# Performance work log

Measured on AMD Instinct MI355X. Metric: run time of the kernel, lower is better.

The kernel has to match this reference:

```python
import jax, jax.numpy as jnp
import numpy as np

N_EMB = 1024
EMB_DIM = 256
COMMITMENT_COST = 0.25


def setup_inputs() -> dict:
    key = jax.random.key(0)
    k1, k2 = jax.random.split(key)
    B = 65536
    x = jax.random.normal(k1, (B, EMB_DIM), dtype=jnp.float32)
    init_bound = 1.0 / 512
    embedding = jax.random.uniform(k2, (N_EMB, EMB_DIM), dtype=jnp.float32,
                                   minval=-init_bound, maxval=init_bound)
    return {"x": x, "embedding": embedding}


def reference(x, embedding):
    B, D = x.shape
    M = embedding.shape[0]
    x_flat = jax.lax.stop_gradient(x)
    # distances[b,m] = ||x_b||^2 + ||e_m||^2 - 2 x_b . e_m  (torch.addmm form)
    distances = (jnp.sum(embedding ** 2, axis=1)[None, :]
                 + jnp.sum(x_flat ** 2, axis=1, keepdims=True)
                 - 2.0 * x_flat @ embedding.T)
    indices = jnp.argmin(distances.astype(jnp.float32), axis=-1)  # [B] int
    quantized = embedding[indices]  # [B, D]

    # commitment loss (quantized detached), masked by non-padding rows
    e_latent = jnp.mean((x - jax.lax.stop_gradient(quantized)) ** 2, axis=-1)  # [B]
    nonpadding = (jnp.sum(jnp.abs(x), axis=-1) > 0).astype(x.dtype)
    loss = COMMITMENT_COST * jnp.sum(e_latent * nonpadding) / jnp.sum(nonpadding)

    # straight-through estimator
    quantized_st = x + jax.lax.stop_gradient(quantized - x)

    # perplexity: avg one-hot probs via bincount (scatter-add, no BxM one-hot)
    counts = jnp.zeros((M,), dtype=jnp.float32).at[indices].add(1.0)
    avg_probs = counts / B
    perplexity = jnp.exp(-jnp.sum(avg_probs * jnp.log(avg_probs + 1e-10)))

    return quantized_st, loss, indices, perplexity
```

## Files before the change

### kernel.cpp

```cpp
#include <hip/hip_runtime.h>

#define BROWS 65536
#define DDIM 256
#define MCODES 1024
#define FLAG_MARGIN 3e-4f
#define RGRP 16
#define NPART 1024

typedef __attribute__((ext_vector_type(8))) _Float16 h8f16;
typedef __attribute__((ext_vector_type(4))) float float4v;

__device__ inline unsigned short f2h_bits(float f) {
  union { _Float16 h; unsigned short u; } cv;
  cv.h = (_Float16)f;
  return cv.u;
}

__global__ __launch_bounds__(256)
void prep_kernel(const float* __restrict__ emb,
                 float* __restrict__ enorm,
                 float* __restrict__ counts, int* __restrict__ nflag,
                 float* __restrict__ loss_extra,
                 unsigned short* __restrict__ eimg, float* __restrict__ embT) {
  int b = blockIdx.x;
  int tid = threadIdx.x;
  if (b < 64) {
    int t = b * 256 + tid;
    if (t < MCODES) counts[t] = 0.0f;
    if (t == 0) *nflag = 0;
    if (t < 2) loss_extra[t] = 0.0f;
    int row = t >> 4;
    int lane = t & 15;
    const float* p = emb + (size_t)row * DDIM;
    int half = (lane >> 3) & 1;
    int j = lane & 7;
    const float* q = p + half * 128 + j;
    float v = q[0];
    float acc = __fmul_rn(v, v);
    #pragma unroll
    for (int i = 1; i < 16; ++i) {
      v = q[i * 8];
      acc = __fadd_rn(acc, __fmul_rn(v, v));
    }
    float o;
    o = __shfl_xor(acc, 1, 64); acc = __fadd_rn(acc, o);
    o = __shfl_xor(acc, 2, 64); acc = __fadd_rn(acc, o);
    o = __shfl_xor(acc, 4, 64); acc = __fadd_rn(acc, o);
    o = __shfl_xor(acc, 8, 64); acc = __fadd_rn(acc, o);
    if (lane == 0) enorm[row] = acc;
  } else if (b < 192) {
    int t = (b - 64) * 256 + tid;
    int lane = t & 63;
    int tile = (t >> 6) & 1;
    int kstep = (t >> 7) & 7;
    int cc = t >> 10;
    int code = cc * 32 + tile * 16 + (lane & 15);
    int kb = kstep * 32 + (lane >> 4) * 8;
    const float* src = emb + (size_t)code * DDIM + kb;
    union { unsigned short u[8]; uint4 v; } out;
    #pragma unroll
    for (int jj = 0; jj < 8; ++jj) out.u[jj] = f2h_bits(src[jj] * 256.0f);
    ((uint4*)eimg)[t] = out.v;
  } else {
    int t = (b - 192) * 256 + tid;
    int base = t * 4;
    int k = base >> 10;
    int m = base & 1023;
    float4 v;
    v.x = emb[(size_t)(m + 0) * DDIM + k];
    v.y = emb[(size_t)(m + 1) * DDIM + k];
    v.z = emb[(size_t)(m + 2) * DDIM + k];
    v.w = emb[(size_t)(m + 3) * DDIM + k];
    *(float4*)&embT[base] = v;
  }
}

__global__ __launch_bounds__(256, 4)
void score_kernel(const float* __restrict__ x, const float* __restrict__ emb,
                  const float* __restrict__ enorm_g,
                  const unsigned short* __restrict__ eimg,
                  int* __restrict__ idx_out, float* __restrict__ out_idxf,
                  float* __restrict__ qout, float* __restrict__ counts,
                  float* __restrict__ loss_part, float* __restrict__ np_part,
                  int* __restrict__ nflag, int* __restrict__ flist) {
  __shared__ __align__(16) unsigned short ebuf[2][8192];
  __shared__ float enorm_s[MCODES];
  __shared__ int lcount;
  __shared__ int lbase;
  __shared__ int lrows[64];
  __shared__ int sidx[64];
  __shared__ unsigned char sflag[64];
  __shared__ float red[8];

  int tid = threadIdx.x;
  int w = tid >> 6;
  int lane = tid & 63;
  int quad = lane >> 4;
  int rowBase = blockIdx.x * 64;
  int waveRow = rowBase + w * 16;

  if (tid == 0) lcount = 0;
  for (int i = tid; i < MCODES; i += 256) enorm_s[i] = enorm_g[i];

  h8f16 xh[8];
  const float* xbase = x + (size_t)(waveRow + (lane & 15)) * DDIM + quad * 8;
  #pragma unroll
  for (int ks = 0; ks < 8; ++ks) {
    const float4* p = (const float4*)(xbase + ks * 32);
    float4 v0 = p[0], v1 = p[1];
    h8f16 h;
    h[0] = (_Float16)v0.x; h[1] = (_Float16)v0.y;
    h[2] = (_Float16)v0.z; h[3] = (_Float16)v0.w;
    h[4] = (_Float16)v1.x; h[5] = (_Float16)v1.y;
    h[6] = (_Float16)v1.z; h[7] = (_Float16)v1.w;
    xh[ks] = h;
  }

  float b1[4], b2[4];
  int i1[4];
  #pragma unroll
  for (int reg = 0; reg < 4; ++reg) { b1[reg] = 3.4e38f; b2[reg] = 3.4e38f; i1[reg] = 0; }

  #define STAGE_CC(ccv, bf) do { \
    const unsigned short* g_ = eimg + (size_t)(ccv) * 8192 + w * 2048 + lane * 8; \
    unsigned short* l_ = &ebuf[(bf)][w * 2048]; \
    _Pragma("unroll") \
    for (int j_ = 0; j_ < 4; ++j_) { \
      __builtin_amdgcn_global_load_lds((const __attribute__((address_space(1))) unsigned int*)(g_ + j_ * 512), \
                                       (__attribute__((address_space(3))) unsigned int*)(l_ + j_ * 512), 16, 0, 0); \
    } \
  } while (0)

  STAGE_CC(0, 0);

  for (int cc = 0; cc < 32; ++cc) {
    int buf = cc & 1;
    __syncthreads();
    if (cc < 31) STAGE_CC(cc + 1, buf ^ 1);

    float4v acc0 = (float4v){0.f, 0.f, 0.f, 0.f};
    float4v acc1 = (float4v){0.f, 0.f, 0.f, 0.f};
    #pragma unroll
    for (int ks = 0; ks < 8; ++ks) {
      h8f16 e0 = *(const h8f16*)&ebuf[buf][ks * 1024 + lane * 8];
      h8f16 e1 = *(const h8f16*)&ebuf[buf][ks * 1024 + 512 + lane * 8];
      acc0 = __builtin_amdgcn_mfma_f32_16x16x32_f16(xh[ks], e0, acc0, 0, 0, 0);
      acc1 = __builtin_amdgcn_mfma_f32_16x16x32_f16(xh[ks], e1, acc1, 0, 0, 0);
    }

    #pragma unroll
    for (int t2 = 0; t2 < 2; ++t2) {
      int m = cc * 32 + t2 * 16 + (lane & 15);
      float en = enorm_s[m];
      #pragma unroll
      for (int reg = 0; reg < 4; ++reg) {
        float av = t2 ? acc1[reg] : acc0[reg];
        float s = __fadd_rn(en, __fmul_rn(-0.0078125f, av));
        if (s < b1[reg]) { b2[reg] = b1[reg]; b1[reg] = s; i1[reg] = m; }
        else { b2[reg] = fminf(b2[reg], s); }
      }
    }
  }

  #pragma unroll
  for (int off = 1; off < 16; off <<= 1) {
    #pragma unroll
    for (int reg = 0; reg < 4; ++reg) {
      float ob1 = __shfl_xor(b1[reg], off, 64);
      float ob2 = __shfl_xor(b2[reg], off, 64);
      int oi = __shfl_xor(i1[reg], off, 64);
      float cb1 = b1[reg], cb2 = b2[reg];
      int ci = i1[reg];
      float nb1, nb2; int ni;
      if (ob1 < cb1)      { nb1 = ob1; ni = oi; nb2 = fminf(cb1, ob2); }
      else if (cb1 < ob1) { nb1 = cb1; ni = ci; nb2 = fminf(ob1, cb2); }
      else                { nb1 = cb1; ni = min(ci, oi); nb2 = cb1; }
      b1[reg] = nb1; b2[reg] = nb2; i1[reg] = ni;
    }
  }

  if ((lane & 15) == 0) {
    #pragma unroll
    for (int reg = 0; reg < 4; ++reg) {
      int row = waveRow + quad * 4 + reg;
      int bi = i1[reg];
      idx_out[row] = bi;
      out_idxf[row] = (float)bi;
      int lr = row - rowBase;
      sidx[lr] = bi;
      int fl = (__fadd_rn(b2[reg], -b1[reg]) <= FLAG_MARGIN) ? 1 : 0;
      sflag[lr] = (unsigned char)fl;
      if (fl) {
        int pp = atomicAdd(&lcount, 1);
        lrows[pp] = row;
      }
    }
  }
  __syncthreads();
  if (tid == 0 && lcount > 0) lbase = atomicAdd(nflag, lcount);
  __syncthreads();
  if (tid < lcount) flist[lbase + tid] = lrows[tid];

  float lsum = 0.0f, nsum = 0.0f;
  for (int it = 0; it < 16; ++it) {
    int lr = w * 16 + it;
    int row = rowBase + lr;
    int id = sidx[lr];
    int fl = sflag[lr];
    float4 xv = ((const float4*)x)[(size_t)row * 64 + lane];
    float4 ev = ((const float4*)emb)[(size_t)id * 64 + lane];
    float4 q;
    q.x = __fadd_rn(xv.x, __fadd_rn(ev.x, -xv.x));
    q.y = __fadd_rn(xv.y, __fadd_rn(ev.y, -xv.y));
    q.z = __fadd_rn(xv.z, __fadd_rn(ev.z, -xv.z));
    q.w = __fadd_rn(xv.w, __fadd_rn(ev.w, -xv.w));
    ((float4*)qout)[(size_t)row * 64 + lane] = q;

    float d0 = xv.x - ev.x, d1 = xv.y - ev.y, d2 = xv.z - ev.z, d3 = xv.w - ev.w;
    float loc = d0 * d0 + d1 * d1 + d2 * d2 + d3 * d3;
    float la = fabsf(xv.x) + fabsf(xv.y) + fabsf(xv.z) + fabsf(xv.w);
    #pragma unroll
    for (int off = 32; off > 0; off >>= 1) {
      loc += __shfl_xor(loc, off, 64);
      la += __shfl_xor(la, off, 64);
    }
    if (lane == 0 && !fl) {
      float np = (la > 0.0f) ? 1.0f : 0.0f;
      lsum += (loc * (1.0f / 256.0f)) * np;
      nsum += np;
      atomicAdd(&counts[id], 1.0f);
    }
  }
  if (lane == 0) { red[w] = lsum; red[4 + w] = nsum; }
  __syncthreads();
  if (tid == 0) {
    loss_part[blockIdx.x] = (red[0] + red[1]) + (red[2] + red[3]);
    np_part[blockIdx.x] = (red[4] + red[5]) + (red[6] + red[7]);
  }
  #undef STAGE_CC
}

__global__ __launch_bounds__(256)
void rescore_kernel(const float* __restrict__ x, const float* __restrict__ emb,
                    const float* __restrict__ embT,
                    const float* __restrict__ enorm,
                    int* __restrict__ idx_out, float* __restrict__ out_idxf,
                    float* __restrict__ qout, float* __restrict__ counts,
                    float* __restrict__ loss_extra,
                    const int* __restrict__ nflag, const int* __restrict__ flist) {
  __shared__ float xs[RGRP][DDIM];
  __shared__ float xnr[RGRP];
  __shared__ int rown[RGRP];
  __shared__ int sbf[RGRP];
  __shared__ float rv[RGRP][256];
  __shared__ int ri[RGRP][256];
  int tid = threadIdx.x;
  int n = nflag[0];

  for (int g = blockIdx.x; g * RGRP < n; g += 1024) {
    int base = g * RGRP;
    int cnt = min(RGRP, n - base);
    __syncthreads();
    if (tid < RGRP) {
      int rr = flist[base + min(tid, cnt - 1)];
      rown[tid] = rr;
    }
    __syncthreads();
    #pragma unroll
    for (int r = 0; r < RGRP; ++r) xs[r][tid] = x[(size_t)rown[r] * DDIM + tid];
    __syncthreads();

    {
      int r = tid >> 4;
      int lane = tid & 15;
      int half = (lane >> 3) & 1;
      int j = lane & 7;
      const float* q = &xs[r][half * 128 + j];
      float v = q[0];
      float acc = __fmul_rn(v, v);
      #pragma unroll
      for (int i = 1; i < 16; ++i) {
        v = q[i * 8];
        acc = __fadd_rn(acc, __fmul_rn(v, v));
      }
      float o;
      o = __shfl_xor(acc, 1, 64); acc = __fadd_rn(acc, o);
      o = __shfl_xor(acc, 2, 64); acc = __fadd_rn(acc, o);
      o = __shfl_xor(acc, 4, 64); acc = __fadd_rn(acc, o);
      o = __shfl_xor(acc, 8, 64); acc = __fadd_rn(acc, o);
      if (lane == 0) xnr[r] = acc;
    }
    __syncthreads();

    float d[4][RGRP];
    #pragma unroll
    for (int c4 = 0; c4 < 4; ++c4)
      #pragma unroll
      for (int r = 0; r < RGRP; ++r) d[c4][r] = 0.0f;

    float e_cur[4][4], e_nxt[4][4];
    #pragma unroll
    for (int kk = 0; kk < 4; ++kk)
      #pragma unroll
      for (int c4 = 0; c4 < 4; ++c4)
        e_cur[kk][c4] = embT[(size_t)kk * 1024 + c4 * 256 + tid];

    for (int k0 = 0; k0 < DDIM; k0 += 4) {
      if (k0 + 4 < DDIM) {
        #pragma unroll
        for (int kk = 0; kk < 4; ++kk)
          #pragma unroll
          for (int c4 = 0; c4 < 4; ++c4)
            e_nxt[kk][c4] = embT[(size_t)(k0 + 4 + kk) * 1024 + c4 * 256 + tid];
      }
      #pragma unroll
      for (int r = 0; r < RGRP; ++r) {
        float4 xv = *(const float4*)&xs[r][k0];
        #pragma unroll
        for (int c4 = 0; c4 < 4; ++c4) {
          d[c4][r] = fmaf(xv.x, e_cur[0][c4], d[c4][r]);
          d[c4][r] = fmaf(xv.y, e_cur[1][c4], d[c4][r]);
          d[c4][r] = fmaf(xv.z, e_cur[2][c4], d[c4][r]);
          d[c4][r] = fmaf(xv.w, e_cur[3][c4], d[c4][r]);
        }
      }
      #pragma unroll
      for (int kk = 0; kk < 4; ++kk)
        #pragma unroll
        for (int c4 = 0; c4 < 4; ++c4)
          e_cur[kk][c4] = e_nxt[kk][c4];
    }

    float b[RGRP]; int bi[RGRP];
    #pragma unroll
    for (int r = 0; r < RGRP; ++r) { b[r] = 3.4e38f; bi[r] = 0; }
    #pragma unroll
    for (int c4 = 0; c4 < 4; ++c4) {
      int m = c4 * 256 + tid;
      float en = enorm[m];
      #pragma unroll
      for (int r = 0; r < RGRP; ++r) {
        float T = __fadd_rn(en, xnr[r]);
        float s = __fadd_rn(T, __fmul_rn(-2.0f, d[c4][r]));
        if (s < b[r] || (s == b[r] && m < bi[r])) { b[r] = s; bi[r] = m; }
      }
    }
    #pragma unroll
    for (int r = 0; r < RGRP; ++r) { rv[r][tid] = b[r]; ri[r][tid] = bi[r]; }
    __syncthreads();
    for (int st = 128; st > 0; st >>= 1) {
      if (tid < st) {
        #pragma unroll
        for (int r = 0; r < RGRP; ++r) {
          float v = rv[r][tid + st]; int m2 = ri[r][tid + st];
          if (v < rv[r][tid] || (v == rv[r][tid] && m2 < ri[r][tid])) { rv[r][tid] = v; ri[r][tid] = m2; }
        }
      }
      __syncthreads();
    }

    if (tid < RGRP) sbf[tid] = ri[tid][0];
    __syncthreads();

    float* laf = (float*)ri;
    #pragma unroll
    for (int r = 0; r < RGRP; ++r) {
      int bf = sbf[r];
      float xv = xs[r][tid];
      float ev = emb[(size_t)bf * DDIM + tid];
      if (r < cnt) {
        float q = __fadd_rn(xv, __fadd_rn(ev, -xv));
        qout[(size_t)rown[r] * DDIM + tid] = q;
      }
      float dd = xv - ev;
      rv[r][tid] = dd * dd;
      laf[r * 256 + tid] = fabsf(xv);
    }
    __syncthreads();
    for (int st = 128; st > 0; st >>= 1) {
      if (tid < st) {
        #pragma unroll
        for (int r = 0; r < RGRP; ++r) {
          rv[r][tid] += rv[r][tid + st];
          laf[r * 256 + tid] += laf[r * 256 + tid + st];
        }
      }
      __syncthreads();
    }
    if (tid < cnt) {
      int bfin = sbf[tid];
      int row = rown[tid];
      float np = (laf[tid * 256] > 0.0f) ? 1.0f : 0.0f;
      atomicAdd(&loss_extra[0], (rv[tid][0] * (1.0f / 256.0f)) * np);
      atomicAdd(&loss_extra[1], np);
      atomicAdd(&counts[bfin], 1.0f);
      idx_out[row] = bfin;
      out_idxf[row] = (float)bfin;
    }
  }
}

__global__ __launch_bounds__(256)
void finalize_kernel(const float* __restrict__ counts,
                     const float* __restrict__ loss_part, const float* __restrict__ np_part,
                     const float* __restrict__ loss_extra,
                     float* __restrict__ out_loss, float* __restrict__ out_perp) {
  __shared__ float red[768];
  int t = threadIdx.x;
  float esum = 0.0f, lsum = 0.0f, nsum = 0.0f;
  for (int m = t; m < MCODES; m += 256) {
    float p = counts[m] * (1.0f / 65536.0f);
    esum += p * logf(p + 1e-10f);
  }
  for (int i = t; i < NPART; i += 256) {
    lsum += loss_part[i];
    nsum += np_part[i];
  }
  red[t] = esum; red[256 + t] = lsum; red[512 + t] = nsum;
  __syncthreads();
  for (int s = 128; s > 0; s >>= 1) {
    if (t < s) {
      red[t] += red[t + s];
      red[256 + t] += red[256 + t + s];
      red[512 + t] += red[512 + t + s];
    }
    __syncthreads();
  }
  if (t == 0) {
    *out_perp = expf(-red[0]);
    float ls = red[256] + loss_extra[0];
    float ns = red[512] + loss_extra[1];
    *out_loss = 0.25f * ls / ns;
  }
}

extern "C" void kernel_launch(void* const* d_in, const int* in_sizes, int n_in,
                              void* d_out, int out_size, void* d_ws, size_t ws_size,
                              hipStream_t stream) {
  (void)in_sizes; (void)n_in; (void)out_size; (void)ws_size;
  const float* x = (const float*)d_in[0];
  const float* emb = (const float*)d_in[1];

  float* out = (float*)d_out;
  float* qst = out;
  float* out_loss = out + 16777216;
  float* out_idxf = out + 16777217;
  float* out_perp = out + 16842753;

  float* ws = (float*)d_ws;
  float* enorm = ws;
  int* idx = (int*)(ws + 1024);
  float* counts = ws + 66560;
  float* lpart = ws + 67584;
  float* npart = ws + 68608;
  float* loss_extra = ws + 69632;
  int* nflag = (int*)(ws + 69634);
  int* flist = (int*)(ws + 69636);
  unsigned short* eimg = (unsigned short*)(ws + 135172);
  float* embT = ws + 266244;

  prep_kernel<<<448, 256, 0, stream>>>(emb, enorm, counts, nflag, loss_extra, eimg, embT);
  score_kernel<<<1024, 256, 0, stream>>>(x, emb, enorm, eimg, idx, out_idxf,
                                         qst, counts, lpart, npart, nflag, flist);
  rescore_kernel<<<1024, 256, 0, stream>>>(x, emb, embT, enorm, idx, out_idxf,
                                           qst, counts, loss_extra, nflag, flist);
  finalize_kernel<<<1, 256, 0, stream>>>(counts, lpart, npart, loss_extra, out_loss, out_perp);
}
```

Before: 242.6 us.

## Split waves 2x2 over rows and code halves to halve LDS codebook reads

Each wave now covers 32 rows and one 16-code half of each 32-code chunk, where before it covered 16 rows and both halves. The intent is that each codebook fragment loaded from LDS feeds two MFMAs, halving LDS read traffic per MFMA. The price is doubled x-fragment registers and per-row best/second-best state, plus an extra shared-memory merge across the two code-half waves with an added barrier. Higher register pressure could reduce occupancy under the 4-blocks launch bound.

```diff
diff --git a/kernel.cpp b/kernel.cpp
--- a/kernel.cpp
+++ b/kernel.cpp
@@ -85,6 +85,8 @@
                   int* __restrict__ nflag, int* __restrict__ flist) {
   __shared__ __align__(16) unsigned short ebuf[2][8192];
   __shared__ float enorm_s[MCODES];
+  __shared__ float sb1[2][64], sb2[2][64];
+  __shared__ int si1[2][64];
   __shared__ int lcount;
   __shared__ int lbase;
   __shared__ int lrows[64];
@@ -97,29 +99,35 @@
   int lane = tid & 63;
   int quad = lane >> 4;
   int rowBase = blockIdx.x * 64;
-  int waveRow = rowBase + w * 16;
+  int waveRow = rowBase + (w & 1) * 32;
+  int ct = w >> 1;
 
   if (tid == 0) lcount = 0;
   for (int i = tid; i < MCODES; i += 256) enorm_s[i] = enorm_g[i];
 
-  h8f16 xh[8];
+  h8f16 xh[2][8];
   const float* xbase = x + (size_t)(waveRow + (lane & 15)) * DDIM + quad * 8;
   #pragma unroll
-  for (int ks = 0; ks < 8; ++ks) {
-    const float4* p = (const float4*)(xbase + ks * 32);
-    float4 v0 = p[0], v1 = p[1];
-    h8f16 h;
-    h[0] = (_Float16)v0.x; h[1] = (_Float16)v0.y;
-    h[2] = (_Float16)v0.z; h[3] = (_Float16)v0.w;
-    h[4] = (_Float16)v1.x; h[5] = (_Float16)v1.y;
-    h[6] = (_Float16)v1.z; h[7] = (_Float16)v1.w;
-    xh[ks] = h;
-  }
-
-  float b1[4], b2[4];
-  int i1[4];
+  for (int rg = 0; rg < 2; ++rg) {
+    #pragma unroll
+    for (int ks = 0; ks < 8; ++ks) {
+      const float4* p = (const float4*)(xbase + rg * 16 * DDIM + ks * 32);
+      float4 v0 = p[0], v1 = p[1];
+      h8f16 h;
+      h[0] = (_Float16)v0.x; h[1] = (_Float16)v0.y;
+      h[2] = (_Float16)v0.z; h[3] = (_Float16)v0.w;
+      h[4] = (_Float16)v1.x; h[5] = (_Float16)v1.y;
+      h[6] = (_Float16)v1.z; h[7] = (_Float16)v1.w;
+      xh[rg][ks] = h;
+    }
+  }
+
+  float b1[2][4], b2[2][4];
+  int i1[2][4];
   #pragma unroll
-  for (int reg = 0; reg < 4; ++reg) { b1[reg] = 3.4e38f; b2[reg] = 3.4e38f; i1[reg] = 0; }
+  for (int rg = 0; rg < 2; ++rg)
+    #pragma unroll
+    for (int reg = 0; reg < 4; ++reg) { b1[rg][reg] = 3.4e38f; b2[rg][reg] = 3.4e38f; i1[rg][reg] = 0; }
 
   #define STAGE_CC(ccv, bf) do { \
     const unsigned short* g_ = eimg + (size_t)(ccv) * 8192 + w * 2048 + lane * 8; \
@@ -142,58 +150,73 @@
     float4v acc1 = (float4v){0.f, 0.f, 0.f, 0.f};
     #pragma unroll
     for (int ks = 0; ks < 8; ++ks) {
-      h8f16 e0 = *(const h8f16*)&ebuf[buf][ks * 1024 + lane * 8];
-      h8f16 e1 = *(const h8f16*)&ebuf[buf][ks * 1024 + 512 + lane * 8];
-      acc0 = __builtin_amdgcn_mfma_f32_16x16x32_f16(xh[ks], e0, acc0, 0, 0, 0);
-      acc1 = __builtin_amdgcn_mfma_f32_16x16x32_f16(xh[ks], e1, acc1, 0, 0, 0);
-    }
-
-    #pragma unroll
-    for (int t2 = 0; t2 < 2; ++t2) {
-      int m = cc * 32 + t2 * 16 + (lane & 15);
-      float en = enorm_s[m];
+      h8f16 e = *(const h8f16*)&ebuf[buf][ks * 1024 + ct * 512 + lane * 8];
+      acc0 = __builtin_amdgcn_mfma_f32_16x16x32_f16(xh[0][ks], e, acc0, 0, 0, 0);
+      acc1 = __builtin_amdgcn_mfma_f32_16x16x32_f16(xh[1][ks], e, acc1, 0, 0, 0);
+    }
+
+    int m = cc * 32 + ct * 16 + (lane & 15);
+    float en = enorm_s[m];
+    #pragma unroll
+    for (int rg = 0; rg < 2; ++rg)
       #pragma unroll
       for (int reg = 0; reg < 4; ++reg) {
-        float av = t2 ? acc1[reg] : acc0[reg];
+        float av = rg ? acc1[reg] : acc0[reg];
         float s = __fadd_rn(en, __fmul_rn(-0.0078125f, av));
-        if (s < b1[reg]) { b2[reg] = b1[reg]; b1[reg] = s; i1[reg] = m; }
-        else { b2[reg] = fminf(b2[reg], s); }
-      }
-    }
+        if (s < b1[rg][reg]) { b2[rg][reg] = b1[rg][reg]; b1[rg][reg] = s; i1[rg][reg] = m; }
+        else { b2[rg][reg] = fminf(b2[rg][reg], s); }
+      }
   }
 
   #pragma unroll
   for (int off = 1; off < 16; off <<= 1) {
     #pragma unroll
-    for (int reg = 0; reg < 4; ++reg) {
-      float ob1 = __shfl_xor(b1[reg], off, 64);
-      float ob2 = __shfl_xor(b2[reg], off, 64);
-      int oi = __shfl_xor(i1[reg], off, 64);
-      float cb1 = b1[reg], cb2 = b2[reg];
-      int ci = i1[reg];
-      float nb1, nb2; int ni;
-      if (ob1 < cb1)      { nb1 = ob1; ni = oi; nb2 = fminf(cb1, ob2); }
-      else if (cb1 < ob1) { nb1 = cb1; ni = ci; nb2 = fminf(ob1, cb2); }
-      else                { nb1 = cb1; ni = min(ci, oi); nb2 = cb1; }
-      b1[reg] = nb1; b2[reg] = nb2; i1[reg] = ni;
-    }
+    for (int rg = 0; rg < 2; ++rg)
+      #pragma unroll
+      for (int reg = 0; reg < 4; ++reg) {
+        float ob1 = __shfl_xor(b1[rg][reg], off, 64);
+        float ob2 = __shfl_xor(b2[rg][reg], off, 64);
+        int oi = __shfl_xor(i1[rg][reg], off, 64);
+        float cb1 = b1[rg][reg], cb2 = b2[rg][reg];
+        int ci = i1[rg][reg];
+        float nb1, nb2; int ni;
+        if (ob1 < cb1)      { nb1 = ob1; ni = oi; nb2 = fminf(cb1, ob2); }
+        else if (cb1 < ob1) { nb1 = cb1; ni = ci; nb2 = fminf(ob1, cb2); }
+        else                { nb1 = cb1; ni = min(ci, oi); nb2 = cb1; }
+        b1[rg][reg] = nb1; b2[rg][reg] = nb2; i1[rg][reg] = ni;
+      }
   }
 
   if ((lane & 15) == 0) {
     #pragma unroll
-    for (int reg = 0; reg < 4; ++reg) {
-      int row = waveRow + quad * 4 + reg;
-      int bi = i1[reg];
-      idx_out[row] = bi;
-      out_idxf[row] = (float)bi;
-      int lr = row - rowBase;
-      sidx[lr] = bi;
-      int fl = (__fadd_rn(b2[reg], -b1[reg]) <= FLAG_MARGIN) ? 1 : 0;
-      sflag[lr] = (unsigned char)fl;
-      if (fl) {
-        int pp = atomicAdd(&lcount, 1);
-        lrows[pp] = row;
-      }
+    for (int rg = 0; rg < 2; ++rg)
+      #pragma unroll
+      for (int reg = 0; reg < 4; ++reg) {
+        int lr = (w & 1) * 32 + rg * 16 + quad * 4 + reg;
+        sb1[ct][lr] = b1[rg][reg];
+        sb2[ct][lr] = b2[rg][reg];
+        si1[ct][lr] = i1[rg][reg];
+      }
+  }
+  __syncthreads();
+
+  if (tid < 64) {
+    float a1 = sb1[0][tid], a2 = sb2[0][tid];
+    float c1 = sb1[1][tid], c2 = sb2[1][tid];
+    int ia = si1[0][tid], ic = si1[1][tid];
+    float f1, f2; int fi;
+    if (a1 < c1)      { f1 = a1; fi = ia; f2 = fminf(a2, c1); }
+    else if (c1 < a1) { f1 = c1; fi = ic; f2 = fminf(c2, a1); }
+    else              { f1 = a1; fi = min(ia, ic); f2 = a1; }
+    int row = rowBase + tid;
+    idx_out[row] = fi;
+    out_idxf[row] = (float)fi;
+    sidx[tid] = fi;
+    int fl = (__fadd_rn(f2, -f1) <= FLAG_MARGIN) ? 1 : 0;
+    sflag[tid] = (unsigned char)fl;
+    if (fl) {
+      int pp = atomicAdd(&lcount, 1);
+      lrows[pp] = row;
     }
   }
   __syncthreads();
```

Measured after the change: 243.6 us. About the same (+0.4%).
